# Performance work log

Measured on AMD Instinct MI355X. Metric: run time of the kernel, lower is better.

Reference implementation:

```python
import jax, jax.numpy as jnp
import numpy as np

N_EMBD = 1024
N_HEAD = 16
HEAD_DIM = 64


def setup_inputs() -> dict:
    key = jax.random.key(0)
    ks = jax.random.split(key, 5)
    x = jax.random.normal(ks[0], (4, 2048, N_EMBD), dtype=jnp.float32)
    # qkv_proj: Linear(n_embd, 3*n_embd) -- torch weight is [out, in]
    W_qkv = jax.random.normal(ks[1], (3 * N_EMBD, N_EMBD), dtype=jnp.float32) * 0.02
    b_qkv = jnp.zeros((3 * N_EMBD,), dtype=jnp.float32)
    W_out = jax.random.normal(ks[2], (N_EMBD, N_EMBD), dtype=jnp.float32) * 0.02
    b_out = jnp.zeros((N_EMBD,), dtype=jnp.float32)
    return {"x": x, "W_qkv": W_qkv, "b_qkv": b_qkv, "W_out": W_out, "b_out": b_out}


def reference(x, W_qkv, b_qkv, W_out, b_out):
    B, S, C = x.shape
    scale = 1.0 / np.sqrt(HEAD_DIM)
    qkv = jnp.einsum('bsc,oc->bso', x, W_qkv) + b_qkv  # [B,S,3C]
    q, k, v = jnp.split(qkv, 3, axis=-1)
    # [B,S,C] -> [B,H,S,Dh]
    def to_heads(t):
        return t.reshape(B, S, N_HEAD, HEAD_DIM).transpose(0, 2, 1, 3)
    q, k, v = to_heads(q), to_heads(k), to_heads(v)
    scores = jnp.einsum('bhqd,bhkd->bhqk', q, k) * scale  # [B,H,S,S]
    causal = jnp.tril(jnp.ones((S, S), dtype=bool))
    scores = jnp.where(causal[None, None], scores, -jnp.inf)
    weights = jax.nn.softmax(scores.astype(jnp.float32), axis=-1).astype(q.dtype)
    y = jnp.einsum('bhqk,bhkd->bhqd', weights, v)  # [B,H,S,Dh]
    y = y.transpose(0, 2, 1, 3).reshape(B, S, C)
    return jnp.einsum('bsc,oc->bso', y, W_out) + b_out
```

## Files before the change

kernel.cpp:

```cpp
#include <hip/hip_runtime.h>
#include <stdint.h>
#include <stddef.h>

typedef __attribute__((ext_vector_type(8))) short short8;
typedef __attribute__((ext_vector_type(4))) float f32x4;
typedef __attribute__((ext_vector_type(16))) float f32x16;
typedef __attribute__((ext_vector_type(4))) unsigned short ushort4v;
typedef __attribute__((ext_vector_type(4))) unsigned int uint4v;

#define SEQ   2048
#define NH    16
#define BATCH 4
#define GK    1024

__device__ __forceinline__ unsigned short f2bf(float f) {
  union { float f; unsigned int u; } v; v.f = f;
  unsigned int u = v.u;
  u += 0x7fffu + ((u >> 16) & 1u);
  return (unsigned short)(u >> 16);
}

__device__ __forceinline__ unsigned cvtpk_bf16(float lo, float hi) {
  unsigned r;
  asm("v_cvt_pk_bf16_f32 %0, %1, %2" : "=v"(r) : "v"(lo), "v"(hi));
  return r;
}

__device__ __forceinline__ void plswap(unsigned &x, unsigned &y) {
#if __has_builtin(__builtin_amdgcn_permlane32_swap)
  auto r = __builtin_amdgcn_permlane32_swap((int)x, (int)y, false, false);
  x = (unsigned)r[0]; y = (unsigned)r[1];
#else
  const unsigned sx = (unsigned)__shfl_xor((int)x, 32);
  const unsigned sy = (unsigned)__shfl_xor((int)y, 32);
  const bool hi = (threadIdx.x & 63) >= 32;
  const unsigned nx = hi ? sy : x;
  const unsigned ny = hi ? y : sx;
  x = nx; y = ny;
#endif
}

__device__ __forceinline__ void gload16(const unsigned short* g, unsigned short* l) {
  __builtin_amdgcn_global_load_lds(
      (const __attribute__((address_space(1))) unsigned int*)g,
      (__attribute__((address_space(3))) unsigned int*)l, 16, 0, 0);
}

__global__ void cvt_all(const float* __restrict__ x, const float* __restrict__ wqkv,
                        const float* __restrict__ wout, unsigned short* __restrict__ dst) {
  const int N1 = (8192 * 1024) / 4, N2 = (3072 * 1024) / 4, N3 = (1024 * 1024) / 4;
  int i = blockIdx.x * blockDim.x + threadIdx.x;
  const int stride = gridDim.x * blockDim.x;
  for (; i < N1 + N2 + N3; i += stride) {
    float4 v;
    if (i < N1)            v = reinterpret_cast<const float4*>(x)[i];
    else if (i < N1 + N2)  v = reinterpret_cast<const float4*>(wqkv)[i - N1];
    else                   v = reinterpret_cast<const float4*>(wout)[i - N1 - N2];
    ushort4v o;
    o[0] = f2bf(v.x); o[1] = f2bf(v.y); o[2] = f2bf(v.z); o[3] = f2bf(v.w);
    reinterpret_cast<ushort4v*>(dst)[i] = o;
  }
}

template<int MODE>
__global__ __launch_bounds__(256, 3)
void gemm_bt(const unsigned short* __restrict__ A,
             const unsigned short* __restrict__ Bw,
             const float* __restrict__ bias,
             unsigned short* __restrict__ q_ws,
             unsigned short* __restrict__ k_ws,
             unsigned short* __restrict__ v_ws,
             float* __restrict__ fout,
             int N)
{
  __shared__ __attribute__((aligned(16))) unsigned short As[128 * 64];
  __shared__ __attribute__((aligned(16))) unsigned short Bs[128 * 64];

  const int t = threadIdx.x;
  const int w = t >> 6, lane = t & 63;
  const int g = lane >> 4, c = lane & 15;
  const int wrow = w >> 1, wcol = w & 1;
  const int m0 = blockIdx.y * 128;
  const int n0 = blockIdx.x * 128;

  const int r8 = lane >> 3;
  const int cgs = (lane & 7) ^ r8;

  const f32x4 fz = {0.f, 0.f, 0.f, 0.f};
  f32x4 acc[4][4];
#pragma unroll
  for (int i = 0; i < 4; ++i)
#pragma unroll
    for (int j = 0; j < 4; ++j) acc[i][j] = fz;

  for (int ks = 0; ks < GK; ks += 64) {
    __syncthreads();
#pragma unroll
    for (int i = 0; i < 4; ++i) {
      const int RB = (i * 4 + w) * 8;
      gload16(A + (size_t)(m0 + RB + r8) * GK + ks + cgs * 8, &As[RB * 64]);
      gload16(Bw + (size_t)(n0 + RB + r8) * GK + ks + cgs * 8, &Bs[RB * 64]);
    }
    __syncthreads();
#pragma unroll
    for (int kk = 0; kk < 2; ++kk) {
      short8 af[4], bfr[4];
#pragma unroll
      for (int mi = 0; mi < 4; ++mi) {
        const int row = wrow * 64 + mi * 16 + c;
        af[mi] = *reinterpret_cast<const short8*>(&As[row * 64 + (((kk * 4 + g) ^ (row & 7)) << 3)]);
      }
#pragma unroll
      for (int ni = 0; ni < 4; ++ni) {
        const int row = wcol * 64 + ni * 16 + c;
        bfr[ni] = *reinterpret_cast<const short8*>(&Bs[row * 64 + (((kk * 4 + g) ^ (row & 7)) << 3)]);
      }
#pragma unroll
      for (int mi = 0; mi < 4; ++mi)
#pragma unroll
        for (int ni = 0; ni < 4; ++ni)
          acc[mi][ni] = __builtin_amdgcn_mfma_f32_16x16x32_bf16(af[mi], bfr[ni], acc[mi][ni], 0, 0, 0);
    }
  }

  if (MODE == 0) {
    const int sec = n0 >> 10;
    unsigned short* dst = (sec == 0) ? q_ws : ((sec == 1) ? k_ws : v_ws);
    const float qsc = (sec == 0) ? (0.125f * 1.44269504f) : 1.0f;
#pragma unroll
    for (int ni = 0; ni < 4; ++ni) {
      const int n = n0 + wcol * 64 + ni * 16 + c;
      const float bb = bias[n];
      const int hh = (n & 1023) >> 6;
      const int d = n & 63;
#pragma unroll
      for (int mi = 0; mi < 4; ++mi) {
#pragma unroll
        for (int r = 0; r < 4; ++r) {
          const int m = m0 + wrow * 64 + mi * 16 + g * 4 + r;
          const int b = m >> 11, s = m & 2047;
          const float val = (acc[mi][ni][r] + bb) * qsc;
          dst[((size_t)((b * NH + hh) * SEQ + s) << 6) + d] = f2bf(val);
        }
      }
    }
  } else {
#pragma unroll
    for (int ni = 0; ni < 4; ++ni) {
      const int n = n0 + wcol * 64 + ni * 16 + c;
      const float bb = bias[n];
#pragma unroll
      for (int mi = 0; mi < 4; ++mi) {
#pragma unroll
        for (int r = 0; r < 4; ++r) {
          const int m = m0 + wrow * 64 + mi * 16 + g * 4 + r;
          fout[(size_t)m * N + n] = acc[mi][ni][r] + bb;
        }
      }
    }
  }
}

__global__ __launch_bounds__(256)
void transpose_v(const unsigned short* __restrict__ v, unsigned short* __restrict__ vt) {
  __shared__ unsigned short T[64][72];
  const int t = threadIdx.x;
  const int bh = blockIdx.y, s0 = blockIdx.x * 64;
  const unsigned short* src = v + ((size_t)bh * SEQ + s0) * 64;
#pragma unroll
  for (int rep = 0; rep < 2; ++rep) {
    const int u = rep * 256 + t;
    const int sr = u >> 3, cg = u & 7;
    const short8 x = *reinterpret_cast<const short8*>(src + (size_t)sr * 64 + cg * 8);
    *reinterpret_cast<short8*>(&T[sr][cg * 8]) = x;
  }
  __syncthreads();
  unsigned short* dst = vt + (size_t)bh * 64 * SEQ + s0;
#pragma unroll
  for (int rep = 0; rep < 2; ++rep) {
    const int u = rep * 256 + t;
    const int d = u >> 3, sc8 = u & 7;
    short8 x;
#pragma unroll
    for (int j = 0; j < 8; ++j) x[j] = (short)T[sc8 * 8 + j][d];
    *reinterpret_cast<short8*>(dst + (size_t)d * SEQ + sc8 * 8) = x;
  }
}

__global__ __launch_bounds__(512, 4)
void attn_fwd12(const unsigned short* __restrict__ q_ws,
                const unsigned short* __restrict__ k_ws,
                const unsigned short* __restrict__ vt_ws,
                unsigned short* __restrict__ y_ws)
{
  __shared__ __attribute__((aligned(16))) unsigned short Ks[3][64 * 64];
  __shared__ __attribute__((aligned(16))) unsigned short Vs[3][64 * 64];

  const int t = threadIdx.x;
  const int w = t >> 6, lane = t & 63;
  const int ql = lane & 31, hi = lane >> 5;
  const int bh = blockIdx.y, b = bh >> 4, h = bh & 15;
  const int jt = (blockIdx.y >= 32) ? (7 - (int)blockIdx.x) : (int)blockIdx.x;
  const int wq0 = jt * 256 + w * 32;
  const int nkt = 4 * jt + 4;

  const int s_row = t >> 3;
  const int s_swz = (t & 7) ^ (s_row & 7);

  const unsigned short* kbase = k_ws + (size_t)bh * SEQ * 64;
  const unsigned short* vbase = vt_ws + (size_t)bh * 64 * SEQ;

  auto stage = [&](int kt, int bi) {
    gload16(kbase + (size_t)kt * 4096 + s_row * 64 + s_swz * 8, &Ks[bi][w * 512]);
    gload16(vbase + (size_t)s_row * SEQ + kt * 64 + s_swz * 8, &Vs[bi][w * 512]);
  };

  const unsigned short* qr = q_ws + ((size_t)bh * SEQ + (wq0 + ql)) * 64;
  short8 qf[4];
#pragma unroll
  for (int ks = 0; ks < 4; ++ks)
    qf[ks] = *reinterpret_cast<const short8*>(qr + ks * 16 + hi * 8);

  f32x16 o0, o1;
#pragma unroll
  for (int i = 0; i < 16; ++i) { o0[i] = 0.f; o1[i] = 0.f; }
  float lsum = 0.f;

  stage(0, 0);
  stage(1, 1);

#pragma unroll 1
  for (int kt = 0; kt < nkt; ++kt) {
    if (kt + 1 < nkt) asm volatile("s_waitcnt lgkmcnt(0) vmcnt(2)" ::: "memory");
    else              asm volatile("s_waitcnt lgkmcnt(0) vmcnt(0)" ::: "memory");
    asm volatile("s_barrier" ::: "memory");
    __builtin_amdgcn_sched_barrier(0);
    if (kt + 2 < nkt) stage(kt + 2, (kt + 2) % 3);

    const int cur = kt % 3;
    const int kt64 = kt * 64;

    if (kt64 <= wq0 + 31) {
      short8 kfl[4], kfh[4];
#pragma unroll
      for (int ks = 0; ks < 4; ++ks) {
        kfl[ks] = *reinterpret_cast<const short8*>(
            &Ks[cur][ql * 64 + (((2 * ks + hi) ^ (ql & 7)) << 3)]);
        kfh[ks] = *reinterpret_cast<const short8*>(
            &Ks[cur][(32 + ql) * 64 + (((2 * ks + hi) ^ (ql & 7)) << 3)]);
      }
      f32x16 s0, s1;
#pragma unroll
      for (int i = 0; i < 16; ++i) { s0[i] = 0.f; s1[i] = 0.f; }
      __builtin_amdgcn_s_setprio(1);
#pragma unroll
      for (int ks = 0; ks < 4; ++ks) {
        s0 = __builtin_amdgcn_mfma_f32_32x32x16_bf16(kfl[ks], qf[ks], s0, 0, 0, 0);
        s1 = __builtin_amdgcn_mfma_f32_32x32x16_bf16(kfh[ks], qf[ks], s1, 0, 0, 0);
      }
      __builtin_amdgcn_s_setprio(0);
      if (kt64 + 63 > wq0) {
        const int gq = wq0 + ql;
#pragma unroll
        for (int r = 0; r < 16; ++r) {
          const int krow = (r & 3) + 8 * (r >> 2) + 4 * hi;
          if (kt64 + krow > gq)      s0[r] = -1e30f;
          if (kt64 + 32 + krow > gq) s1[r] = -1e30f;
        }
      }
      float psum = 0.f;
      unsigned W[16];
#pragma unroll
      for (int half = 0; half < 2; ++half) {
#pragma unroll
        for (int gr = 0; gr < 4; ++gr) {
          const float p0 = __builtin_amdgcn_exp2f(half ? s1[gr * 4 + 0] : s0[gr * 4 + 0]);
          const float p1 = __builtin_amdgcn_exp2f(half ? s1[gr * 4 + 1] : s0[gr * 4 + 1]);
          const float p2 = __builtin_amdgcn_exp2f(half ? s1[gr * 4 + 2] : s0[gr * 4 + 2]);
          const float p3 = __builtin_amdgcn_exp2f(half ? s1[gr * 4 + 3] : s0[gr * 4 + 3]);
          psum += (p0 + p1) + (p2 + p3);
          W[half * 8 + 2 * gr]     = cvtpk_bf16(p0, p1);
          W[half * 8 + 2 * gr + 1] = cvtpk_bf16(p2, p3);
        }
      }
      lsum += psum;
      short8 pa[4];
#pragma unroll
      for (int q4 = 0; q4 < 4; ++q4) {
        unsigned a0 = W[q4 * 4 + 0], a1 = W[q4 * 4 + 2];
        unsigned b0 = W[q4 * 4 + 1], b1 = W[q4 * 4 + 3];
        plswap(a0, a1);
        plswap(b0, b1);
        uint4v pk; pk[0] = a0; pk[1] = b0; pk[2] = a1; pk[3] = b1;
        pa[q4] = __builtin_bit_cast(short8, pk);
      }
      __builtin_amdgcn_s_setprio(1);
#pragma unroll
      for (int ks = 0; ks < 4; ++ks) {
        const short8 vfl = *reinterpret_cast<const short8*>(
            &Vs[cur][ql * 64 + (((2 * ks + hi) ^ (ql & 7)) << 3)]);
        const short8 vfh = *reinterpret_cast<const short8*>(
            &Vs[cur][(32 + ql) * 64 + (((2 * ks + hi) ^ (ql & 7)) << 3)]);
        o0 = __builtin_amdgcn_mfma_f32_32x32x16_bf16(pa[ks], vfl, o0, 0, 0, 0);
        o1 = __builtin_amdgcn_mfma_f32_32x32x16_bf16(pa[ks], vfh, o1, 0, 0, 0);
      }
      __builtin_amdgcn_s_setprio(0);
    }
  }

  lsum += __shfl_xor(lsum, 32);
  const float linv = 1.f / lsum;
#pragma unroll
  for (int r = 0; r < 16; ++r) {
    const int qq = (r & 3) + 8 * (r >> 2) + 4 * hi;
    const float lr = __shfl(linv, qq);
    const size_t rowo = ((size_t)b * SEQ + (wq0 + qq)) * 1024 + h * 64;
    y_ws[rowo + ql]      = f2bf(o0[r] * lr);
    y_ws[rowo + 32 + ql] = f2bf(o1[r] * lr);
  }
}

extern "C" void kernel_launch(void* const* d_in, const int* in_sizes, int n_in,
                              void* d_out, int out_size, void* d_ws, size_t ws_size,
                              hipStream_t stream)
{
  (void)in_sizes; (void)n_in; (void)out_size; (void)ws_size;
  const float* x     = (const float*)d_in[0];
  const float* W_qkv = (const float*)d_in[1];
  const float* b_qkv = (const float*)d_in[2];
  const float* W_out = (const float*)d_in[3];
  const float* b_out = (const float*)d_in[4];
  float* out = (float*)d_out;

  unsigned short* ws      = (unsigned short*)d_ws;
  unsigned short* x_bf    = ws;
  unsigned short* wqkv_bf = x_bf    + (size_t)8192 * 1024;
  unsigned short* wout_bf = wqkv_bf + (size_t)3072 * 1024;
  unsigned short* q_ws    = wout_bf + (size_t)1024 * 1024;
  unsigned short* k_ws    = q_ws    + (size_t)64 * SEQ * 64;
  unsigned short* v_ws    = k_ws    + (size_t)64 * SEQ * 64;
  unsigned short* y_ws    = v_ws    + (size_t)64 * SEQ * 64;
  unsigned short* vt_ws   = x_bf;

  cvt_all<<<2048, 256, 0, stream>>>(x, W_qkv, W_out, x_bf);

  gemm_bt<0><<<dim3(24, 64), 256, 0, stream>>>(x_bf, wqkv_bf, b_qkv, q_ws, k_ws, v_ws, nullptr, 3072);
  transpose_v<<<dim3(SEQ / 64, 64), 256, 0, stream>>>(v_ws, vt_ws);
  attn_fwd12<<<dim3(8, 64), 512, 0, stream>>>(q_ws, k_ws, vt_ws, y_ws);
  gemm_bt<1><<<dim3(8, 64), 256, 0, stream>>>(y_ws, wout_bf, b_out, nullptr, nullptr, nullptr, out, 1024);
}
```

Baseline: 170.6 us.

## Stage 128-key K/V tiles with double buffering in attention kernel

The attention loop now loads 128 keys of K and V^T per stage into a two-slot LDS ring instead of 64 keys into a three-slot ring. Each iteration processes two 64-key subtiles, so there are half as many barriers and waitcnt points. The V^T tile uses a 16-way XOR swizzle to suit its wider rows. In exchange, prefetch depth drops to one stage with a full vmcnt(0) wait, which may expose load latency. LDS use grows from 48KB to 64KB per block, which may reduce occupancy.

```diff
diff --git a/kernel.cpp b/kernel.cpp
--- a/kernel.cpp
+++ b/kernel.cpp
@@ -188,13 +188,13 @@
 }
 
 __global__ __launch_bounds__(512, 4)
-void attn_fwd12(const unsigned short* __restrict__ q_ws,
+void attn_fwd13(const unsigned short* __restrict__ q_ws,
                 const unsigned short* __restrict__ k_ws,
                 const unsigned short* __restrict__ vt_ws,
                 unsigned short* __restrict__ y_ws)
 {
-  __shared__ __attribute__((aligned(16))) unsigned short Ks[3][64 * 64];
-  __shared__ __attribute__((aligned(16))) unsigned short Vs[3][64 * 64];
+  __shared__ __attribute__((aligned(16))) unsigned short Ks[2][128 * 64];
+  __shared__ __attribute__((aligned(16))) unsigned short Vs[2][64 * 128];
 
   const int t = threadIdx.x;
   const int w = t >> 6, lane = t & 63;
@@ -202,17 +202,23 @@
   const int bh = blockIdx.y, b = bh >> 4, h = bh & 15;
   const int jt = (blockIdx.y >= 32) ? (7 - (int)blockIdx.x) : (int)blockIdx.x;
   const int wq0 = jt * 256 + w * 32;
-  const int nkt = 4 * jt + 4;
-
-  const int s_row = t >> 3;
-  const int s_swz = (t & 7) ^ (s_row & 7);
+  const int nit = 2 * jt + 2;
+
+  const int kr  = w * 8 + (lane >> 3);
+  const int ksw = (lane & 7) ^ (kr & 7);
+  const int vr  = w * 4 + (lane >> 4);
+  const int vsw = (lane & 15) ^ (vr & 15);
 
   const unsigned short* kbase = k_ws + (size_t)bh * SEQ * 64;
   const unsigned short* vbase = vt_ws + (size_t)bh * 64 * SEQ;
 
-  auto stage = [&](int kt, int bi) {
-    gload16(kbase + (size_t)kt * 4096 + s_row * 64 + s_swz * 8, &Ks[bi][w * 512]);
-    gload16(vbase + (size_t)s_row * SEQ + kt * 64 + s_swz * 8, &Vs[bi][w * 512]);
+  auto stage = [&](int it2, int bi) {
+    const unsigned short* kp = kbase + (size_t)it2 * 8192;
+    gload16(kp + (size_t)kr * 64 + ksw * 8,        &Ks[bi][w * 512]);
+    gload16(kp + (size_t)(kr + 64) * 64 + ksw * 8, &Ks[bi][4096 + w * 512]);
+    const unsigned short* vp = vbase + (size_t)it2 * 128;
+    gload16(vp + (size_t)vr * SEQ + vsw * 8,        &Vs[bi][w * 512]);
+    gload16(vp + (size_t)(vr + 32) * SEQ + vsw * 8, &Vs[bi][4096 + w * 512]);
   };
 
   const unsigned short* qr = q_ws + ((size_t)bh * SEQ + (wq0 + ql)) * 64;
@@ -227,84 +233,82 @@
   float lsum = 0.f;
 
   stage(0, 0);
-  stage(1, 1);
 
 #pragma unroll 1
-  for (int kt = 0; kt < nkt; ++kt) {
-    if (kt + 1 < nkt) asm volatile("s_waitcnt lgkmcnt(0) vmcnt(2)" ::: "memory");
-    else              asm volatile("s_waitcnt lgkmcnt(0) vmcnt(0)" ::: "memory");
+  for (int it = 0; it < nit; ++it) {
+    asm volatile("s_waitcnt lgkmcnt(0) vmcnt(0)" ::: "memory");
     asm volatile("s_barrier" ::: "memory");
     __builtin_amdgcn_sched_barrier(0);
-    if (kt + 2 < nkt) stage(kt + 2, (kt + 2) % 3);
-
-    const int cur = kt % 3;
-    const int kt64 = kt * 64;
-
-    if (kt64 <= wq0 + 31) {
-      short8 kfl[4], kfh[4];
-#pragma unroll
-      for (int ks = 0; ks < 4; ++ks) {
-        kfl[ks] = *reinterpret_cast<const short8*>(
-            &Ks[cur][ql * 64 + (((2 * ks + hi) ^ (ql & 7)) << 3)]);
-        kfh[ks] = *reinterpret_cast<const short8*>(
-            &Ks[cur][(32 + ql) * 64 + (((2 * ks + hi) ^ (ql & 7)) << 3)]);
-      }
-      f32x16 s0, s1;
-#pragma unroll
-      for (int i = 0; i < 16; ++i) { s0[i] = 0.f; s1[i] = 0.f; }
-      __builtin_amdgcn_s_setprio(1);
-#pragma unroll
-      for (int ks = 0; ks < 4; ++ks) {
-        s0 = __builtin_amdgcn_mfma_f32_32x32x16_bf16(kfl[ks], qf[ks], s0, 0, 0, 0);
-        s1 = __builtin_amdgcn_mfma_f32_32x32x16_bf16(kfh[ks], qf[ks], s1, 0, 0, 0);
-      }
-      __builtin_amdgcn_s_setprio(0);
-      if (kt64 + 63 > wq0) {
-        const int gq = wq0 + ql;
-#pragma unroll
-        for (int r = 0; r < 16; ++r) {
-          const int krow = (r & 3) + 8 * (r >> 2) + 4 * hi;
-          if (kt64 + krow > gq)      s0[r] = -1e30f;
-          if (kt64 + 32 + krow > gq) s1[r] = -1e30f;
-        }
-      }
-      float psum = 0.f;
-      unsigned W[16];
-#pragma unroll
-      for (int half = 0; half < 2; ++half) {
-#pragma unroll
-        for (int gr = 0; gr < 4; ++gr) {
-          const float p0 = __builtin_amdgcn_exp2f(half ? s1[gr * 4 + 0] : s0[gr * 4 + 0]);
-          const float p1 = __builtin_amdgcn_exp2f(half ? s1[gr * 4 + 1] : s0[gr * 4 + 1]);
-          const float p2 = __builtin_amdgcn_exp2f(half ? s1[gr * 4 + 2] : s0[gr * 4 + 2]);
-          const float p3 = __builtin_amdgcn_exp2f(half ? s1[gr * 4 + 3] : s0[gr * 4 + 3]);
-          psum += (p0 + p1) + (p2 + p3);
-          W[half * 8 + 2 * gr]     = cvtpk_bf16(p0, p1);
-          W[half * 8 + 2 * gr + 1] = cvtpk_bf16(p2, p3);
-        }
-      }
-      lsum += psum;
-      short8 pa[4];
-#pragma unroll
-      for (int q4 = 0; q4 < 4; ++q4) {
-        unsigned a0 = W[q4 * 4 + 0], a1 = W[q4 * 4 + 2];
-        unsigned b0 = W[q4 * 4 + 1], b1 = W[q4 * 4 + 3];
-        plswap(a0, a1);
-        plswap(b0, b1);
-        uint4v pk; pk[0] = a0; pk[1] = b0; pk[2] = a1; pk[3] = b1;
-        pa[q4] = __builtin_bit_cast(short8, pk);
-      }
-      __builtin_amdgcn_s_setprio(1);
-#pragma unroll
-      for (int ks = 0; ks < 4; ++ks) {
-        const short8 vfl = *reinterpret_cast<const short8*>(
-            &Vs[cur][ql * 64 + (((2 * ks + hi) ^ (ql & 7)) << 3)]);
-        const short8 vfh = *reinterpret_cast<const short8*>(
-            &Vs[cur][(32 + ql) * 64 + (((2 * ks + hi) ^ (ql & 7)) << 3)]);
-        o0 = __builtin_amdgcn_mfma_f32_32x32x16_bf16(pa[ks], vfl, o0, 0, 0, 0);
-        o1 = __builtin_amdgcn_mfma_f32_32x32x16_bf16(pa[ks], vfh, o1, 0, 0, 0);
-      }
-      __builtin_amdgcn_s_setprio(0);
+    if (it + 1 < nit) stage(it + 1, (it + 1) & 1);
+    const int cur = it & 1;
+
+#pragma unroll
+    for (int hh2 = 0; hh2 < 2; ++hh2) {
+      const int kt64 = it * 128 + hh2 * 64;
+      if (kt64 <= wq0 + 31) {
+        short8 kfl[4], kfh[4];
+#pragma unroll
+        for (int ks = 0; ks < 4; ++ks) {
+          const int co = ((2 * ks + hi) ^ (ql & 7)) << 3;
+          kfl[ks] = *reinterpret_cast<const short8*>(&Ks[cur][(hh2 * 64 + ql) * 64 + co]);
+          kfh[ks] = *reinterpret_cast<const short8*>(&Ks[cur][(hh2 * 64 + 32 + ql) * 64 + co]);
+        }
+        f32x16 s0, s1;
+#pragma unroll
+        for (int i = 0; i < 16; ++i) { s0[i] = 0.f; s1[i] = 0.f; }
+        __builtin_amdgcn_s_setprio(1);
+#pragma unroll
+        for (int ks = 0; ks < 4; ++ks) {
+          s0 = __builtin_amdgcn_mfma_f32_32x32x16_bf16(kfl[ks], qf[ks], s0, 0, 0, 0);
+          s1 = __builtin_amdgcn_mfma_f32_32x32x16_bf16(kfh[ks], qf[ks], s1, 0, 0, 0);
+        }
+        __builtin_amdgcn_s_setprio(0);
+        if (kt64 + 63 > wq0) {
+          const int gq = wq0 + ql;
+#pragma unroll
+          for (int r = 0; r < 16; ++r) {
+            const int krow = (r & 3) + 8 * (r >> 2) + 4 * hi;
+            if (kt64 + krow > gq)      s0[r] = -1e30f;
+            if (kt64 + 32 + krow > gq) s1[r] = -1e30f;
+          }
+        }
+        float psum = 0.f;
+        unsigned W[16];
+#pragma unroll
+        for (int half = 0; half < 2; ++half) {
+#pragma unroll
+          for (int gr = 0; gr < 4; ++gr) {
+            const float p0 = __builtin_amdgcn_exp2f(half ? s1[gr * 4 + 0] : s0[gr * 4 + 0]);
+            const float p1 = __builtin_amdgcn_exp2f(half ? s1[gr * 4 + 1] : s0[gr * 4 + 1]);
+            const float p2 = __builtin_amdgcn_exp2f(half ? s1[gr * 4 + 2] : s0[gr * 4 + 2]);
+            const float p3 = __builtin_amdgcn_exp2f(half ? s1[gr * 4 + 3] : s0[gr * 4 + 3]);
+            psum += (p0 + p1) + (p2 + p3);
+            W[half * 8 + 2 * gr]     = cvtpk_bf16(p0, p1);
+            W[half * 8 + 2 * gr + 1] = cvtpk_bf16(p2, p3);
+          }
+        }
+        lsum += psum;
+        short8 pa[4];
+#pragma unroll
+        for (int q4 = 0; q4 < 4; ++q4) {
+          unsigned a0 = W[q4 * 4 + 0], a1 = W[q4 * 4 + 2];
+          unsigned b0 = W[q4 * 4 + 1], b1 = W[q4 * 4 + 3];
+          plswap(a0, a1);
+          plswap(b0, b1);
+          uint4v pk; pk[0] = a0; pk[1] = b0; pk[2] = a1; pk[3] = b1;
+          pa[q4] = __builtin_bit_cast(short8, pk);
+        }
+        __builtin_amdgcn_s_setprio(1);
+#pragma unroll
+        for (int ks = 0; ks < 4; ++ks) {
+          const int vo = ((hh2 * 8 + 2 * ks + hi) ^ (ql & 15)) << 3;
+          const short8 vfl = *reinterpret_cast<const short8*>(&Vs[cur][ql * 128 + vo]);
+          const short8 vfh = *reinterpret_cast<const short8*>(&Vs[cur][(32 + ql) * 128 + vo]);
+          o0 = __builtin_amdgcn_mfma_f32_32x32x16_bf16(pa[ks], vfl, o0, 0, 0, 0);
+          o1 = __builtin_amdgcn_mfma_f32_32x32x16_bf16(pa[ks], vfh, o1, 0, 0, 0);
+        }
+        __builtin_amdgcn_s_setprio(0);
+      }
     }
   }
 
@@ -346,6 +350,6 @@
 
   gemm_bt<0><<<dim3(24, 64), 256, 0, stream>>>(x_bf, wqkv_bf, b_qkv, q_ws, k_ws, v_ws, nullptr, 3072);
   transpose_v<<<dim3(SEQ / 64, 64), 256, 0, stream>>>(v_ws, vt_ws);
-  attn_fwd12<<<dim3(8, 64), 512, 0, stream>>>(q_ws, k_ws, vt_ws, y_ws);
+  attn_fwd13<<<dim3(8, 64), 512, 0, stream>>>(q_ws, k_ws, vt_ws, y_ws);
   gemm_bt<1><<<dim3(8, 64), 256, 0, stream>>>(y_ws, wout_bf, b_out, nullptr, nullptr, nullptr, out, 1024);
 }
```

New measurement: 175.1 us. +2.7%, slower.
